# Kernel optimization log

Measured on AMD Instinct MI355X. Metric: run time of the kernel, lower is better.

Reference implementation:

```python
import jax, jax.numpy as jnp
import numpy as np

N = 262144       # batch rows
C = 256          # in_channels
K = 256          # uint8 code range


def setup_inputs() -> dict:
    key = jax.random.key(0)
    k1, k2, k3, k4 = jax.random.split(key, 4)
    left = jax.random.randint(k1, (N, C), 0, K, dtype=jnp.int32)
    right = jax.random.randint(k2, (N, C), 0, K, dtype=jnp.int32)
    # per-channel 256x256 lookup tables: white_table[c][l, r] -> new code in [0, 256)
    white_table = jax.random.randint(k3, (C, K, K), 0, K, dtype=jnp.int32)
    # per-channel last-layer codebook: last_codebook[c][1][code] -> float
    codebook = jax.random.normal(k4, (C, K), dtype=jnp.float32)
    return {"left": left, "right": right, "white_table": white_table, "codebook": codebook}


def reference(left, right, white_table, codebook):
    # Fused equivalent of the per-channel python loop:
    #   for c: codes[:, c] = white_table[c][left[:, c], right[:, c]]
    #   out[:, c]  = codebook[c][codes[:, c]]
    ch = jnp.arange(C, dtype=jnp.int32)[None, :]          # [1, C] broadcasts vs [N, C]
    codes = white_table[ch, left, right]                   # [N, C] int32 gather
    out = codebook[ch, codes]                              # [N, C] float32 gather
    return out
```

## Files before the change

kernel.cpp:

```cpp
#include <hip/hip_runtime.h>
#include <stdint.h>

#define CCH 256
#define KK  256

typedef int   i32x4 __attribute__((ext_vector_type(4)));
typedef float f32x4 __attribute__((ext_vector_type(4)));
typedef unsigned short u16x4 __attribute__((ext_vector_type(4)));
typedef unsigned short u16x8 __attribute__((ext_vector_type(8)));

__global__ __launch_bounds__(256) void compress_table_kernel(
    const int4* __restrict__ t, uchar4* __restrict__ o, int n4) {
  int i = blockIdx.x * 256 + threadIdx.x;
  if (i < n4) {
    int4 v = t[i];
    o[i] = make_uchar4((unsigned char)v.x, (unsigned char)v.y,
                       (unsigned char)v.z, (unsigned char)v.w);
  }
}

__global__ __launch_bounds__(256, 4) void transpose_pack_kernel(
    const i32x4* __restrict__ L4, const i32x4* __restrict__ R4,
    unsigned short* __restrict__ LRt, int n0_base, int nslice) {
  __shared__ unsigned short tile[64 * 260];
  const int tn   = blockIdx.x;
  const int gn0  = n0_base + tn * 64;
  const int lane = threadIdx.x & 63;
  const int wid  = threadIdx.x >> 6;

#pragma unroll
  for (int p = 0; p < 16; ++p) {
    const int r = p * 4 + wid;
    const size_t gi = (size_t)(gn0 + r) * 64 + lane;
    i32x4 Lv = L4[gi];
    i32x4 Rv = R4[gi];
    u16x4 w;
    w[0] = (unsigned short)((Lv[0] << 8) | Rv[0]);
    w[1] = (unsigned short)((Lv[1] << 8) | Rv[1]);
    w[2] = (unsigned short)((Lv[2] << 8) | Rv[2]);
    w[3] = (unsigned short)((Lv[3] << 8) | Rv[3]);
    const int col = (lane * 4) ^ (((r >> 3) & 7) << 2);
    *(u16x4*)&tile[r * 260 + col] = w;
  }
  __syncthreads();

#pragma unroll
  for (int pb = 0; pb < 8; ++pb) {
    const int ch = pb * 32 + (threadIdx.x >> 3);
    const int n8 = threadIdx.x & 7;
    u16x8 v;
#pragma unroll
    for (int j = 0; j < 8; ++j) {
      const int r = n8 * 8 + j;
      v[j] = tile[r * 260 + (ch ^ (n8 << 2))];
    }
    *(u16x8*)&LRt[(size_t)ch * nslice + tn * 64 + n8 * 8] = v;
  }
}

__global__ __launch_bounds__(512, 4) void code_gather_kernel(
    const unsigned short* __restrict__ LRt, const unsigned char* __restrict__ tab8,
    unsigned char* __restrict__ codes, int nslice) {
  __shared__ unsigned char tabs[KK * KK];
  const int c   = blockIdx.x & (CCH - 1);
  const int sub = blockIdx.x >> 8;
  {
    const int4* src = (const int4*)(tab8 + (size_t)c * (KK * KK));
    int4* dst = (int4*)tabs;
#pragma unroll
    for (int i = 0; i < 8; ++i) dst[threadIdx.x + 512 * i] = src[threadIdx.x + 512 * i];
  }
  __syncthreads();
  const size_t base = (size_t)c * nslice + (size_t)sub * 16384;
  const u16x8* __restrict__ in   = (const u16x8*)(LRt + base);
  uint2*       __restrict__ outp = (uint2*)(codes + base);
  u16x8 v0 = in[          threadIdx.x];
  u16x8 v1 = in[ 512 +    threadIdx.x];
  u16x8 v2 = in[1024 +    threadIdx.x];
  u16x8 v3 = in[1536 +    threadIdx.x];
#define PACK8(v, slot)                                                          \
  {                                                                             \
    unsigned lo = (unsigned)tabs[v[0]] | ((unsigned)tabs[v[1]] << 8) |          \
                  ((unsigned)tabs[v[2]] << 16) | ((unsigned)tabs[v[3]] << 24);  \
    unsigned hi = (unsigned)tabs[v[4]] | ((unsigned)tabs[v[5]] << 8) |          \
                  ((unsigned)tabs[v[6]] << 16) | ((unsigned)tabs[v[7]] << 24);  \
    outp[slot * 512 + threadIdx.x] = make_uint2(lo, hi);                        \
  }
  PACK8(v0, 0) PACK8(v1, 1) PACK8(v2, 2) PACK8(v3, 3)
#undef PACK8
}

__global__ __launch_bounds__(256) void codebook_transpose_kernel(
    const unsigned char* __restrict__ codes, const float* __restrict__ cb,
    float* __restrict__ out, int n0_base, int nslice) {
  __shared__ float cbs[16 * KK];
  __shared__ unsigned ctd[16 * 66];
  const int ntiles = nslice >> 8;
  const int tn = blockIdx.x % ntiles;
  const int tc = blockIdx.x / ntiles;
  const int c0 = tc * 16;
  {
    const f32x4* cbg = (const f32x4*)(cb + (size_t)c0 * KK);
    f32x4* cbl = (f32x4*)cbs;
#pragma unroll
    for (int i = 0; i < 4; ++i) cbl[threadIdx.x + 256 * i] = cbg[threadIdx.x + 256 * i];
  }
  {
    const int cc = threadIdx.x >> 4, l16 = threadIdx.x & 15;
    const unsigned* row =
        (const unsigned*)(codes + (size_t)(c0 + cc) * nslice + (size_t)tn * 256);
#pragma unroll
    for (int q = 0; q < 4; ++q) ctd[cc * 66 + q * 16 + l16] = row[q * 16 + l16];
  }
  __syncthreads();
  const int cc = threadIdx.x & 15, nn4 = threadIdx.x >> 4;
  const float* cbrow = cbs + cc * KK;
  float* obase = out + (size_t)(n0_base + tn * 256) * CCH + c0 + cc;
#pragma unroll
  for (int p = 0; p < 4; ++p) {
    const int d = p * 16 + nn4;
    const unsigned c4v = ctd[cc * 66 + d];
#pragma unroll
    for (int k = 0; k < 4; ++k) {
      const float val = cbrow[(c4v >> (8 * k)) & 255u];
      __builtin_nontemporal_store(val, obase + (size_t)(d * 4 + k) * CCH);
    }
  }
}

#define ROWS_PER_BLOCK 512
#define NGROUPS 16
#define GCH (CCH / NGROUPS)

template <typename TabT>
__global__ __launch_bounds__(256, 8) void gather_kernel(
    const i32x4* __restrict__ left, const i32x4* __restrict__ right,
    const TabT* __restrict__ tab, const float* __restrict__ cb,
    f32x4* __restrict__ out, int nrows) {
  __shared__ float cbs[GCH * KK];
  const int g     = blockIdx.x & (NGROUPS - 1);
  const int chunk = blockIdx.x / NGROUPS;
  const int q     = threadIdx.x & 3;
  const int rsub  = threadIdx.x >> 2;
  {
    const f32x4* cbg = (const f32x4*)(cb + (size_t)(g * GCH) * KK);
    f32x4* cbl = (f32x4*)cbs;
#pragma unroll
    for (int i = 0; i < 4; ++i) cbl[threadIdx.x + i * 256] = cbg[threadIdx.x + i * 256];
  }
  __syncthreads();
  const int cbase  = g * GCH + q * 4;
  const TabT* t0   = tab + (size_t)cbase * (KK * KK);
  const int vecoff = g * 4 + q;
  const float* cq  = cbs + (q * 4) * KK;
  const int rbase = chunk * ROWS_PER_BLOCK;
#pragma unroll
  for (int it = 0; it < ROWS_PER_BLOCK / 32; ++it) {
    const int r0 = rbase + it * 32 + rsub;
    if (r0 >= nrows) break;
    const unsigned v0 = (unsigned)r0 * 64u + (unsigned)vecoff;
    i32x4 L0 = left[v0];
    i32x4 R0 = right[v0];
    unsigned c0 = (unsigned)t0[          (unsigned)(L0[0] * KK + R0[0])];
    unsigned c1 = (unsigned)t0[ 65536u + (unsigned)(L0[1] * KK + R0[1])];
    unsigned c2 = (unsigned)t0[131072u + (unsigned)(L0[2] * KK + R0[2])];
    unsigned c3 = (unsigned)t0[196608u + (unsigned)(L0[3] * KK + R0[3])];
    f32x4 o;
    o[0] = cq[       c0];
    o[1] = cq[KK   + c1];
    o[2] = cq[2*KK + c2];
    o[3] = cq[3*KK + c3];
    out[v0] = o;
  }
}

extern "C" void kernel_launch(void* const* d_in, const int* in_sizes, int n_in,
                              void* d_out, int out_size, void* d_ws, size_t ws_size,
                              hipStream_t stream) {
  const int*   left  = (const int*)d_in[0];
  const int*   right = (const int*)d_in[1];
  const int*   wt    = (const int*)d_in[2];
  const float* cb    = (const float*)d_in[3];
  float* out = (float*)d_out;

  const int nrows = in_sizes[0] / CCH;
  const int tab_elems = CCH * KK * KK;
  const size_t tab_bytes = (size_t)tab_elems;

  int S = 0;
  for (int s = 1; s <= 16; s <<= 1) {
    if (nrows % (s * 16384)) continue;
    size_t need = tab_bytes + (size_t)768 * (size_t)(nrows / s);
    if (need <= ws_size) { S = s; break; }
  }

  if (S) {
    unsigned char* tab8 = (unsigned char*)d_ws;
    int n4 = tab_elems / 4;
    compress_table_kernel<<<n4 / 256, 256, 0, stream>>>(
        (const int4*)wt, (uchar4*)tab8, n4);

    const int nslice = nrows / S;
    unsigned short* LRt = (unsigned short*)((char*)d_ws + tab_bytes);
    unsigned char* codes = (unsigned char*)d_ws + tab_bytes + (size_t)512 * nslice;

    for (int h = 0; h < S; ++h) {
      const int n0 = h * nslice;
      transpose_pack_kernel<<<nslice / 64, 256, 0, stream>>>(
          (const i32x4*)left, (const i32x4*)right, LRt, n0, nslice);
      code_gather_kernel<<<(nslice / 16384) * CCH, 512, 0, stream>>>(
          LRt, tab8, codes, nslice);
      codebook_transpose_kernel<<<(nslice / 256) * 16, 256, 0, stream>>>(
          codes, cb, out, n0, nslice);
    }
  } else if (ws_size >= tab_bytes) {
    unsigned char* tab8 = (unsigned char*)d_ws;
    int n4 = tab_elems / 4;
    compress_table_kernel<<<n4 / 256, 256, 0, stream>>>(
        (const int4*)wt, (uchar4*)tab8, n4);
    const int blocks = ((nrows + ROWS_PER_BLOCK - 1) / ROWS_PER_BLOCK) * NGROUPS;
    gather_kernel<unsigned char><<<blocks, 256, 0, stream>>>(
        (const i32x4*)left, (const i32x4*)right, tab8, cb, (f32x4*)out, nrows);
  } else {
    const int blocks = ((nrows + ROWS_PER_BLOCK - 1) / ROWS_PER_BLOCK) * NGROUPS;
    gather_kernel<int><<<blocks, 256, 0, stream>>>(
        (const i32x4*)left, (const i32x4*)right, wt, cb, (f32x4*)out, nrows);
  }
}
```

Measured before the change: 756.9 us.

## Enlarge tiles in transpose, code-gather and codebook stages for more reuse

```diff
diff --git a/kernel.cpp b/kernel.cpp
--- a/kernel.cpp
+++ b/kernel.cpp
@@ -19,19 +19,19 @@
   }
 }
 
-__global__ __launch_bounds__(256, 4) void transpose_pack_kernel(
+__global__ __launch_bounds__(512, 4) void transpose_pack_kernel(
     const i32x4* __restrict__ L4, const i32x4* __restrict__ R4,
     unsigned short* __restrict__ LRt, int n0_base, int nslice) {
-  __shared__ unsigned short tile[64 * 260];
-  const int tn   = blockIdx.x;
-  const int gn0  = n0_base + tn * 64;
-  const int lane = threadIdx.x & 63;
-  const int wid  = threadIdx.x >> 6;
+  __shared__ unsigned short tile[128 * 260];
+  const int tn  = blockIdx.x;
+  const int gn0 = n0_base + tn * 128;
 
 #pragma unroll
   for (int p = 0; p < 16; ++p) {
-    const int r = p * 4 + wid;
-    const size_t gi = (size_t)(gn0 + r) * 64 + lane;
+    const int idx = p * 512 + (int)threadIdx.x;
+    const int r   = idx >> 6;
+    const int cq  = idx & 63;
+    const size_t gi = (size_t)(gn0 + r) * 64 + cq;
     i32x4 Lv = L4[gi];
     i32x4 Rv = R4[gi];
     u16x4 w;
@@ -39,22 +39,25 @@
     w[1] = (unsigned short)((Lv[1] << 8) | Rv[1]);
     w[2] = (unsigned short)((Lv[2] << 8) | Rv[2]);
     w[3] = (unsigned short)((Lv[3] << 8) | Rv[3]);
-    const int col = (lane * 4) ^ (((r >> 3) & 7) << 2);
+    const int col = (cq * 4) ^ (((r >> 3) & 15) << 2);
     *(u16x4*)&tile[r * 260 + col] = w;
   }
   __syncthreads();
 
-#pragma unroll
-  for (int pb = 0; pb < 8; ++pb) {
-    const int ch = pb * 32 + (threadIdx.x >> 3);
-    const int n8 = threadIdx.x & 7;
+  const int wv = threadIdx.x >> 6;
+  const int l  = threadIdx.x & 63;
+  const int m  = l & 15;
+  const int c4 = l >> 4;
+#pragma unroll
+  for (int p = 0; p < 8; ++p) {
+    const int ch = wv * 32 + p * 4 + c4;
     u16x8 v;
 #pragma unroll
     for (int j = 0; j < 8; ++j) {
-      const int r = n8 * 8 + j;
-      v[j] = tile[r * 260 + (ch ^ (n8 << 2))];
-    }
-    *(u16x8*)&LRt[(size_t)ch * nslice + tn * 64 + n8 * 8] = v;
+      const int r = m * 8 + j;
+      v[j] = tile[r * 260 + (ch ^ (m << 2))];
+    }
+    *(u16x8*)&LRt[(size_t)ch * nslice + (size_t)tn * 128 + m * 8] = v;
   }
 }
 
@@ -64,20 +67,27 @@
   __shared__ unsigned char tabs[KK * KK];
   const int c   = blockIdx.x & (CCH - 1);
   const int sub = blockIdx.x >> 8;
+  const size_t base = (size_t)c * nslice + (size_t)sub * 32768;
+  const u16x8* __restrict__ in   = (const u16x8*)(LRt + base);
+  uint2*       __restrict__ outp = (uint2*)(codes + base);
+
+  u16x8 v0 = in[0 * 512 + threadIdx.x];
+  u16x8 v1 = in[1 * 512 + threadIdx.x];
+  u16x8 v2 = in[2 * 512 + threadIdx.x];
+  u16x8 v3 = in[3 * 512 + threadIdx.x];
+  u16x8 v4 = in[4 * 512 + threadIdx.x];
+  u16x8 v5 = in[5 * 512 + threadIdx.x];
+  u16x8 v6 = in[6 * 512 + threadIdx.x];
+  u16x8 v7 = in[7 * 512 + threadIdx.x];
+
   {
     const int4* src = (const int4*)(tab8 + (size_t)c * (KK * KK));
     int4* dst = (int4*)tabs;
 #pragma unroll
-    for (int i = 0; i < 8; ++i) dst[threadIdx.x + 512 * i] = src[threadIdx.x + 512 * i];
-  }
-  __syncthreads();
-  const size_t base = (size_t)c * nslice + (size_t)sub * 16384;
-  const u16x8* __restrict__ in   = (const u16x8*)(LRt + base);
-  uint2*       __restrict__ outp = (uint2*)(codes + base);
-  u16x8 v0 = in[          threadIdx.x];
-  u16x8 v1 = in[ 512 +    threadIdx.x];
-  u16x8 v2 = in[1024 +    threadIdx.x];
-  u16x8 v3 = in[1536 +    threadIdx.x];
+    for (int i = 0; i < 8; ++i) dst[i * 512 + threadIdx.x] = src[i * 512 + threadIdx.x];
+  }
+  __syncthreads();
+
 #define PACK8(v, slot)                                                          \
   {                                                                             \
     unsigned lo = (unsigned)tabs[v[0]] | ((unsigned)tabs[v[1]] << 8) |          \
@@ -87,43 +97,53 @@
     outp[slot * 512 + threadIdx.x] = make_uint2(lo, hi);                        \
   }
   PACK8(v0, 0) PACK8(v1, 1) PACK8(v2, 2) PACK8(v3, 3)
+  PACK8(v4, 4) PACK8(v5, 5) PACK8(v6, 6) PACK8(v7, 7)
 #undef PACK8
 }
 
-__global__ __launch_bounds__(256) void codebook_transpose_kernel(
+__global__ __launch_bounds__(512, 2) void codebook_transpose_kernel(
     const unsigned char* __restrict__ codes, const float* __restrict__ cb,
     float* __restrict__ out, int n0_base, int nslice) {
-  __shared__ float cbs[16 * KK];
-  __shared__ unsigned ctd[16 * 66];
-  const int ntiles = nslice >> 8;
-  const int tn = blockIdx.x % ntiles;
-  const int tc = blockIdx.x / ntiles;
-  const int c0 = tc * 16;
+  __shared__ float    cbs[64 * KK];
+  __shared__ unsigned ctile[64 * 129];
+  const int cg = blockIdx.x & 3;
+  const int tn = blockIdx.x >> 2;
+  const int c0 = cg * 64;
+
   {
     const f32x4* cbg = (const f32x4*)(cb + (size_t)c0 * KK);
     f32x4* cbl = (f32x4*)cbs;
 #pragma unroll
-    for (int i = 0; i < 4; ++i) cbl[threadIdx.x + 256 * i] = cbg[threadIdx.x + 256 * i];
-  }
-  {
-    const int cc = threadIdx.x >> 4, l16 = threadIdx.x & 15;
-    const unsigned* row =
-        (const unsigned*)(codes + (size_t)(c0 + cc) * nslice + (size_t)tn * 256);
-#pragma unroll
-    for (int q = 0; q < 4; ++q) ctd[cc * 66 + q * 16 + l16] = row[q * 16 + l16];
-  }
-  __syncthreads();
-  const int cc = threadIdx.x & 15, nn4 = threadIdx.x >> 4;
-  const float* cbrow = cbs + cc * KK;
-  float* obase = out + (size_t)(n0_base + tn * 256) * CCH + c0 + cc;
-#pragma unroll
-  for (int p = 0; p < 4; ++p) {
-    const int d = p * 16 + nn4;
-    const unsigned c4v = ctd[cc * 66 + d];
+    for (int i = 0; i < 8; ++i) cbl[i * 512 + threadIdx.x] = cbg[i * 512 + threadIdx.x];
+  }
+  {
+    const int cc = threadIdx.x >> 3;
+    const int s  = threadIdx.x & 7;
+    const unsigned char* srow = codes + (size_t)(c0 + cc) * nslice + (size_t)tn * 512;
 #pragma unroll
     for (int k = 0; k < 4; ++k) {
-      const float val = cbrow[(c4v >> (8 * k)) & 255u];
-      __builtin_nontemporal_store(val, obase + (size_t)(d * 4 + k) * CCH);
+      uint4 val = *(const uint4*)(srow + s * 16 + k * 128);
+      const int d0 = cc * 129 + k * 32 + s * 4;
+      ctile[d0 + 0] = val.x;
+      ctile[d0 + 1] = val.y;
+      ctile[d0 + 2] = val.z;
+      ctile[d0 + 3] = val.w;
+    }
+  }
+  __syncthreads();
+
+  const int l = threadIdx.x & 63;
+  const int w = threadIdx.x >> 6;
+  const float* cbrow = cbs + l * KK;
+  float* ob = out + (size_t)(n0_base + tn * 512) * CCH + c0 + l;
+#pragma unroll
+  for (int it = 0; it < 16; ++it) {
+    const int n4 = it * 8 + w;
+    const unsigned cw = ctile[l * 129 + n4];
+#pragma unroll
+    for (int k = 0; k < 4; ++k) {
+      const float vv = cbrow[(cw >> (8 * k)) & 255u];
+      __builtin_nontemporal_store(vv, ob + (size_t)(n4 * 4 + k) * CCH);
     }
   }
 }
@@ -188,8 +208,8 @@
   const size_t tab_bytes = (size_t)tab_elems;
 
   int S = 0;
-  for (int s = 1; s <= 16; s <<= 1) {
-    if (nrows % (s * 16384)) continue;
+  for (int s = 1; s <= 8; s <<= 1) {
+    if (nrows % (s * 32768)) continue;
     size_t need = tab_bytes + (size_t)768 * (size_t)(nrows / s);
     if (need <= ws_size) { S = s; break; }
   }
@@ -206,11 +226,11 @@
 
     for (int h = 0; h < S; ++h) {
       const int n0 = h * nslice;
-      transpose_pack_kernel<<<nslice / 64, 256, 0, stream>>>(
+      transpose_pack_kernel<<<nslice / 128, 512, 0, stream>>>(
           (const i32x4*)left, (const i32x4*)right, LRt, n0, nslice);
-      code_gather_kernel<<<(nslice / 16384) * CCH, 512, 0, stream>>>(
+      code_gather_kernel<<<(nslice / 32768) * CCH, 512, 0, stream>>>(
           LRt, tab8, codes, nslice);
-      codebook_transpose_kernel<<<(nslice / 256) * 16, 256, 0, stream>>>(
+      codebook_transpose_kernel<<<(nslice / 512) * 4, 512, 0, stream>>>(
           codes, cb, out, n0, nslice);
     }
   } else if (ws_size >= tab_bytes) {
```

After: 709.8 us. -6.2%, faster.

## Retile pack/gather/codebook pipeline with blocked intermediate layout and register prefetch

Applied to the files above, without the earlier changes.

```diff
diff --git a/kernel.cpp b/kernel.cpp
--- a/kernel.cpp
+++ b/kernel.cpp
@@ -19,112 +19,156 @@
   }
 }
 
-__global__ __launch_bounds__(256, 4) void transpose_pack_kernel(
+__global__ __launch_bounds__(256, 3) void transpose_pack_kernel(
     const i32x4* __restrict__ L4, const i32x4* __restrict__ R4,
-    unsigned short* __restrict__ LRt, int n0_base, int nslice) {
-  __shared__ unsigned short tile[64 * 260];
-  const int tn   = blockIdx.x;
-  const int gn0  = n0_base + tn * 64;
-  const int lane = threadIdx.x & 63;
-  const int wid  = threadIdx.x >> 6;
-
-#pragma unroll
-  for (int p = 0; p < 16; ++p) {
-    const int r = p * 4 + wid;
-    const size_t gi = (size_t)(gn0 + r) * 64 + lane;
-    i32x4 Lv = L4[gi];
-    i32x4 Rv = R4[gi];
-    u16x4 w;
-    w[0] = (unsigned short)((Lv[0] << 8) | Rv[0]);
-    w[1] = (unsigned short)((Lv[1] << 8) | Rv[1]);
-    w[2] = (unsigned short)((Lv[2] << 8) | Rv[2]);
-    w[3] = (unsigned short)((Lv[3] << 8) | Rv[3]);
-    const int col = (lane * 4) ^ (((r >> 3) & 7) << 2);
-    *(u16x4*)&tile[r * 260 + col] = w;
-  }
-  __syncthreads();
-
-#pragma unroll
-  for (int pb = 0; pb < 8; ++pb) {
-    const int ch = pb * 32 + (threadIdx.x >> 3);
-    const int n8 = threadIdx.x & 7;
-    u16x8 v;
-#pragma unroll
-    for (int j = 0; j < 8; ++j) {
-      const int r = n8 * 8 + j;
-      v[j] = tile[r * 260 + (ch ^ (n8 << 2))];
-    }
-    *(u16x8*)&LRt[(size_t)ch * nslice + tn * 64 + n8 * 8] = v;
+    unsigned short* __restrict__ LRtT, int n0_base, int nslice) {
+  __shared__ unsigned short tile[32 * 260];
+  const int T     = 8;
+  const int tile0 = blockIdx.x * T;
+  const int tid   = threadIdx.x;
+  const int w     = tid >> 6;
+  const int lq    = tid & 63;
+
+  i32x4 Lb[8], Rb[8];
+  {
+    const size_t rowbase = (size_t)(n0_base + tile0 * 32);
+#pragma unroll
+    for (int p = 0; p < 8; ++p) {
+      const size_t gi = (rowbase + p * 4 + w) * 64 + lq;
+      Lb[p] = L4[gi];
+      Rb[p] = R4[gi];
+    }
+  }
+
+#pragma unroll 1
+  for (int t = 0; t < T; ++t) {
+#pragma unroll
+    for (int p = 0; p < 8; ++p) {
+      u16x4 pk;
+      pk[0] = (unsigned short)((Lb[p][0] << 8) | Rb[p][0]);
+      pk[1] = (unsigned short)((Lb[p][1] << 8) | Rb[p][1]);
+      pk[2] = (unsigned short)((Lb[p][2] << 8) | Rb[p][2]);
+      pk[3] = (unsigned short)((Lb[p][3] << 8) | Rb[p][3]);
+      *(u16x4*)&tile[(p * 4 + w) * 260 + lq * 4] = pk;
+    }
+    if (t + 1 < T) {
+      const size_t rowbase = (size_t)(n0_base + (tile0 + t + 1) * 32);
+#pragma unroll
+      for (int p = 0; p < 8; ++p) {
+        const size_t gi = (rowbase + p * 4 + w) * 64 + lq;
+        Lb[p] = L4[gi];
+        Rb[p] = R4[gi];
+      }
+    }
+    asm volatile("s_waitcnt lgkmcnt(0)" ::: "memory");
+    __builtin_amdgcn_s_barrier();
+
+    {
+      unsigned short col[32];
+#pragma unroll
+      for (int r = 0; r < 32; ++r) col[r] = tile[r * 260 + tid];
+      u16x8 s0, s1, s2, s3;
+#pragma unroll
+      for (int j = 0; j < 8; ++j) {
+        s0[j] = col[j];
+        s1[j] = col[8 + j];
+        s2[j] = col[16 + j];
+        s3[j] = col[24 + j];
+      }
+      unsigned short* dst = LRtT + ((size_t)(tile0 + t) * CCH + tid) * 32;
+      *(u16x8*)(dst + 0)  = s0;
+      *(u16x8*)(dst + 8)  = s1;
+      *(u16x8*)(dst + 16) = s2;
+      *(u16x8*)(dst + 24) = s3;
+    }
+    asm volatile("s_waitcnt lgkmcnt(0)" ::: "memory");
+    __builtin_amdgcn_s_barrier();
   }
 }
 
 __global__ __launch_bounds__(512, 4) void code_gather_kernel(
-    const unsigned short* __restrict__ LRt, const unsigned char* __restrict__ tab8,
+    const unsigned short* __restrict__ LRtT, const unsigned char* __restrict__ tab8,
     unsigned char* __restrict__ codes, int nslice) {
   __shared__ unsigned char tabs[KK * KK];
   const int c   = blockIdx.x & (CCH - 1);
   const int sub = blockIdx.x >> 8;
+  const int tid = threadIdx.x;
+  const int tbase = sub * 1024;
+
+  u16x8 v[8];
+#pragma unroll
+  for (int i = 0; i < 8; ++i) {
+    const size_t a =
+        ((size_t)(tbase + i * 128 + (tid >> 2)) * CCH + c) * 32 + (tid & 3) * 8;
+    v[i] = *(const u16x8*)(LRtT + a);
+  }
   {
     const int4* src = (const int4*)(tab8 + (size_t)c * (KK * KK));
     int4* dst = (int4*)tabs;
 #pragma unroll
-    for (int i = 0; i < 8; ++i) dst[threadIdx.x + 512 * i] = src[threadIdx.x + 512 * i];
+    for (int i = 0; i < 8; ++i) dst[i * 512 + tid] = src[i * 512 + tid];
   }
   __syncthreads();
-  const size_t base = (size_t)c * nslice + (size_t)sub * 16384;
-  const u16x8* __restrict__ in   = (const u16x8*)(LRt + base);
-  uint2*       __restrict__ outp = (uint2*)(codes + base);
-  u16x8 v0 = in[          threadIdx.x];
-  u16x8 v1 = in[ 512 +    threadIdx.x];
-  u16x8 v2 = in[1024 +    threadIdx.x];
-  u16x8 v3 = in[1536 +    threadIdx.x];
-#define PACK8(v, slot)                                                          \
-  {                                                                             \
-    unsigned lo = (unsigned)tabs[v[0]] | ((unsigned)tabs[v[1]] << 8) |          \
-                  ((unsigned)tabs[v[2]] << 16) | ((unsigned)tabs[v[3]] << 24);  \
-    unsigned hi = (unsigned)tabs[v[4]] | ((unsigned)tabs[v[5]] << 8) |          \
-                  ((unsigned)tabs[v[6]] << 16) | ((unsigned)tabs[v[7]] << 24);  \
-    outp[slot * 512 + threadIdx.x] = make_uint2(lo, hi);                        \
-  }
-  PACK8(v0, 0) PACK8(v1, 1) PACK8(v2, 2) PACK8(v3, 3)
-#undef PACK8
-}
-
-__global__ __launch_bounds__(256) void codebook_transpose_kernel(
+
+  uint2* outp = (uint2*)(codes + (size_t)c * nslice + (size_t)sub * 32768);
+#pragma unroll
+  for (int i = 0; i < 8; ++i) {
+    unsigned lo = (unsigned)tabs[v[i][0]] | ((unsigned)tabs[v[i][1]] << 8) |
+                  ((unsigned)tabs[v[i][2]] << 16) | ((unsigned)tabs[v[i][3]] << 24);
+    unsigned hi = (unsigned)tabs[v[i][4]] | ((unsigned)tabs[v[i][5]] << 8) |
+                  ((unsigned)tabs[v[i][6]] << 16) | ((unsigned)tabs[v[i][7]] << 24);
+    outp[i * 512 + tid] = make_uint2(lo, hi);
+  }
+}
+
+__global__ __launch_bounds__(512, 6) void codebook_transpose_kernel(
     const unsigned char* __restrict__ codes, const float* __restrict__ cb,
     float* __restrict__ out, int n0_base, int nslice) {
-  __shared__ float cbs[16 * KK];
-  __shared__ unsigned ctd[16 * 66];
-  const int ntiles = nslice >> 8;
-  const int tn = blockIdx.x % ntiles;
-  const int tc = blockIdx.x / ntiles;
-  const int c0 = tc * 16;
+  __shared__ float    cbs[32 * KK];
+  __shared__ unsigned ctd[32 * 65];
+  const int cg = blockIdx.x & 7;
+  const int tn = blockIdx.x >> 3;
+  const int c0 = cg * 32;
+  const int tid = threadIdx.x;
+
   {
     const f32x4* cbg = (const f32x4*)(cb + (size_t)c0 * KK);
     f32x4* cbl = (f32x4*)cbs;
 #pragma unroll
-    for (int i = 0; i < 4; ++i) cbl[threadIdx.x + 256 * i] = cbg[threadIdx.x + 256 * i];
-  }
-  {
-    const int cc = threadIdx.x >> 4, l16 = threadIdx.x & 15;
-    const unsigned* row =
-        (const unsigned*)(codes + (size_t)(c0 + cc) * nslice + (size_t)tn * 256);
-#pragma unroll
-    for (int q = 0; q < 4; ++q) ctd[cc * 66 + q * 16 + l16] = row[q * 16 + l16];
+    for (int i = 0; i < 4; ++i) cbl[i * 512 + tid] = cbg[i * 512 + tid];
+  }
+  {
+    const int cc = tid >> 4;
+    const int s  = tid & 15;
+    const uint4 val = *(const uint4*)(codes + (size_t)(c0 + cc) * nslice +
+                                      (size_t)tn * 256 + s * 16);
+    const int d0 = cc * 65 + s * 4;
+    ctd[d0 + 0] = val.x;
+    ctd[d0 + 1] = val.y;
+    ctd[d0 + 2] = val.z;
+    ctd[d0 + 3] = val.w;
   }
   __syncthreads();
-  const int cc = threadIdx.x & 15, nn4 = threadIdx.x >> 4;
-  const float* cbrow = cbs + cc * KK;
-  float* obase = out + (size_t)(n0_base + tn * 256) * CCH + c0 + cc;
-#pragma unroll
-  for (int p = 0; p < 4; ++p) {
-    const int d = p * 16 + nn4;
-    const unsigned c4v = ctd[cc * 66 + d];
-#pragma unroll
-    for (int k = 0; k < 4; ++k) {
-      const float val = cbrow[(c4v >> (8 * k)) & 255u];
-      __builtin_nontemporal_store(val, obase + (size_t)(d * 4 + k) * CCH);
-    }
+
+  const int cq = tid & 7;
+  const int nb = tid >> 3;
+  const unsigned cw0 = ctd[(cq * 4 + 0) * 65 + nb];
+  const unsigned cw1 = ctd[(cq * 4 + 1) * 65 + nb];
+  const unsigned cw2 = ctd[(cq * 4 + 2) * 65 + nb];
+  const unsigned cw3 = ctd[(cq * 4 + 3) * 65 + nb];
+  const float* b0 = cbs + (cq * 4 + 0) * KK;
+  const float* b1 = cbs + (cq * 4 + 1) * KK;
+  const float* b2 = cbs + (cq * 4 + 2) * KK;
+  const float* b3 = cbs + (cq * 4 + 3) * KK;
+  float* ob = out + (size_t)(n0_base + tn * 256 + nb * 4) * CCH + c0 + cq * 4;
+#pragma unroll
+  for (int k = 0; k < 4; ++k) {
+    f32x4 o;
+    o[0] = b0[(cw0 >> (8 * k)) & 255u];
+    o[1] = b1[(cw1 >> (8 * k)) & 255u];
+    o[2] = b2[(cw2 >> (8 * k)) & 255u];
+    o[3] = b3[(cw3 >> (8 * k)) & 255u];
+    __builtin_nontemporal_store(o, (f32x4*)(ob + (size_t)k * CCH));
   }
 }
 
@@ -188,8 +232,8 @@
   const size_t tab_bytes = (size_t)tab_elems;
 
   int S = 0;
-  for (int s = 1; s <= 16; s <<= 1) {
-    if (nrows % (s * 16384)) continue;
+  for (int s = 1; s <= 8; s <<= 1) {
+    if (nrows % (s * 32768)) continue;
     size_t need = tab_bytes + (size_t)768 * (size_t)(nrows / s);
     if (need <= ws_size) { S = s; break; }
   }
@@ -201,16 +245,16 @@
         (const int4*)wt, (uchar4*)tab8, n4);
 
     const int nslice = nrows / S;
-    unsigned short* LRt = (unsigned short*)((char*)d_ws + tab_bytes);
+    unsigned short* LRtT = (unsigned short*)((char*)d_ws + tab_bytes);
     unsigned char* codes = (unsigned char*)d_ws + tab_bytes + (size_t)512 * nslice;
 
     for (int h = 0; h < S; ++h) {
       const int n0 = h * nslice;
-      transpose_pack_kernel<<<nslice / 64, 256, 0, stream>>>(
-          (const i32x4*)left, (const i32x4*)right, LRt, n0, nslice);
-      code_gather_kernel<<<(nslice / 16384) * CCH, 512, 0, stream>>>(
-          LRt, tab8, codes, nslice);
-      codebook_transpose_kernel<<<(nslice / 256) * 16, 256, 0, stream>>>(
+      transpose_pack_kernel<<<nslice / 256, 256, 0, stream>>>(
+          (const i32x4*)left, (const i32x4*)right, LRtT, n0, nslice);
+      code_gather_kernel<<<(nslice / 32768) * CCH, 512, 0, stream>>>(
+          LRtT, tab8, codes, nslice);
+      codebook_transpose_kernel<<<(nslice / 256) * 8, 512, 0, stream>>>(
           codes, cb, out, n0, nslice);
     }
   } else if (ws_size >= tab_bytes) {
```

Result: faster. 728.5 us (-3.8%).
